# Kernel tuning notes

Hardware: AMD Instinct MI355X
Metric: run time of the kernel (lower is better)

## Reference

```python
import jax, jax.numpy as jnp
import numpy as np

N, T = 1024, 32
D_FEAT, GATE_START, GATE_END = 158, 158, 221
D_MODEL = 256
T_NHEAD, S_NHEAD = 4, 2
BETA = 5.0
LN_EPS = 1e-5


def _ln(x, g, b):
    mu = jnp.mean(x, axis=-1, keepdims=True)
    var = jnp.mean(jnp.square(x - mu), axis=-1, keepdims=True)
    return (x - mu) * jax.lax.rsqrt(var + LN_EPS) * g + b


def _pos_enc(t, d):
    pos = jnp.arange(t, dtype=jnp.float32)[:, None]
    div = jnp.exp(jnp.arange(0, d, 2, dtype=jnp.float32) * (-np.log(10000.0) / d))
    pe = jnp.zeros((t, d), dtype=jnp.float32)
    pe = pe.at[:, 0::2].set(jnp.sin(pos * div))
    pe = pe.at[:, 1::2].set(jnp.cos(pos * div))
    return pe


def _mha(xn, qw, kw, vw, nhead, temperature):
    # xn: [B, S, D] (already layer-normed); attention over axis S
    B, S, D = xn.shape
    dh = D // nhead
    q = (xn @ qw.T).reshape(B, S, nhead, dh)
    k = (xn @ kw.T).reshape(B, S, nhead, dh)
    v = (xn @ vw.T).reshape(B, S, nhead, dh)
    scores = jnp.einsum('bshd,bthd->bhst', q, k) / temperature
    a = jax.nn.softmax(scores, axis=-1)
    return jnp.einsum('bhst,bthd->bshd', a, v).reshape(B, S, D)


def _block(x, qw, kw, vw, n1g, n1b, n2g, n2b, f1w, f1b, f2w, f2b, nhead, temperature):
    xn = _ln(x, n1g, n1b)
    xt = xn + _mha(xn, qw, kw, vw, nhead, temperature)
    xt = _ln(xt, n2g, n2b)
    ffn = jnp.maximum(xt @ f1w.T + f1b, 0.0) @ f2w.T + f2b
    return xt + ffn


def _forward(x, gate_w, gate_b, proj_w, proj_b,
             tq, tk, tv, tn1g, tn1b, tn2g, tn2b, tf1w, tf1b, tf2w, tf2b,
             sq, sk, sv, sn1g, sn1b, sn2g, sn2b, sf1w, sf1b, sf2w, sf2b,
             temp_w, out_w, out_b):
    src = x[:, :, :GATE_START]                     # [N, T, d_feat]
    gate_in = x[:, -1, GATE_START:GATE_END]        # [N, d_gate]
    gate = D_FEAT * jax.nn.softmax((gate_in @ gate_w.T + gate_b) / BETA, axis=-1)
    src = src * gate[:, None, :]
    z = src @ proj_w.T + proj_b                    # [N, T, d_model]
    z = z + _pos_enc(z.shape[1], D_MODEL)
    # TAttention: attend over time, unscaled scores (temperature=1)
    z = _block(z, tq, tk, tv, tn1g, tn1b, tn2g, tn2b, tf1w, tf1b, tf2w, tf2b,
               T_NHEAD, 1.0)
    # SAttention: attend over stocks, temperature = sqrt(d_model/nhead)
    zs = _block(z.swapaxes(0, 1), sq, sk, sv, sn1g, sn1b, sn2g, sn2b,
                sf1w, sf1b, sf2w, sf2b, S_NHEAD, float(np.sqrt(D_MODEL / S_NHEAD)))
    z = zs.swapaxes(0, 1)                          # [N, T, d_model]
    # TemporalAttention pooling
    h = z @ temp_w.T
    lam = jax.nn.softmax(jnp.einsum('ntd,nd->nt', h, h[:, -1, :]), axis=1)
    pooled = jnp.einsum('nt,ntd->nd', lam, z)
    return (pooled @ out_w.T + out_b).squeeze(-1)  # [N]


def setup_inputs() -> dict:
    key = jax.random.key(0)
    ks = iter(jax.random.split(key, 32))
    s = 0.02
    d, f, g = D_MODEL, D_FEAT, GATE_END - GATE_START
    inp = {
        'x': jax.random.normal(next(ks), (N, T, GATE_END), dtype=jnp.float32),
        'gate_w': jax.random.normal(next(ks), (f, g)) * s,
        'gate_b': jnp.zeros((f,)),
        'proj_w': jax.random.normal(next(ks), (d, f)) * s,
        'proj_b': jnp.zeros((d,)),
        'tq': jax.random.normal(next(ks), (d, d)) * s,
        'tk': jax.random.normal(next(ks), (d, d)) * s,
        'tv': jax.random.normal(next(ks), (d, d)) * s,
        'tn1g': jnp.ones((d,)), 'tn1b': jnp.zeros((d,)),
        'tn2g': jnp.ones((d,)), 'tn2b': jnp.zeros((d,)),
        'tf1w': jax.random.normal(next(ks), (d, d)) * s, 'tf1b': jnp.zeros((d,)),
        'tf2w': jax.random.normal(next(ks), (d, d)) * s, 'tf2b': jnp.zeros((d,)),
        'sq': jax.random.normal(next(ks), (d, d)) * s,
        'sk': jax.random.normal(next(ks), (d, d)) * s,
        'sv': jax.random.normal(next(ks), (d, d)) * s,
        'sn1g': jnp.ones((d,)), 'sn1b': jnp.zeros((d,)),
        'sn2g': jnp.ones((d,)), 'sn2b': jnp.zeros((d,)),
        'sf1w': jax.random.normal(next(ks), (d, d)) * s, 'sf1b': jnp.zeros((d,)),
        'sf2w': jax.random.normal(next(ks), (d, d)) * s, 'sf2b': jnp.zeros((d,)),
        'temp_w': jax.random.normal(next(ks), (d, d)) * s,
        'out_w': jax.random.normal(next(ks), (1, d)) * s,
        'out_b': jnp.zeros((1,)),
    }
    return {k: v.astype(jnp.float32) for k, v in inp.items()}


def reference(x, gate_w, gate_b, proj_w, proj_b,
              tq, tk, tv, tn1g, tn1b, tn2g, tn2b, tf1w, tf1b, tf2w, tf2b,
              sq, sk, sv, sn1g, sn1b, sn2g, sn2b, sf1w, sf1b, sf2w, sf2b,
              temp_w, out_w, out_b):
    return _forward(x, gate_w, gate_b, proj_w, proj_b,
                    tq, tk, tv, tn1g, tn1b, tn2g, tn2b, tf1w, tf1b, tf2w, tf2b,
                    sq, sk, sv, sn1g, sn1b, sn2g, sn2b, sf1w, sf1b, sf2w, sf2b,
                    temp_w, out_w, out_b)
```

## Files before the change

kernel.cpp:

```cpp
#include <hip/hip_runtime.h>
#include <math.h>

#define NB   1024
#define TSEQ 32
#define DM   256
#define DF   158
#define GDIM 63
#define XROW 221

typedef unsigned short u16;
typedef __attribute__((ext_vector_type(8))) __bf16 bf16x8;
typedef __attribute__((ext_vector_type(4))) float f32x4;
#define MFMA16(a,b,c) __builtin_amdgcn_mfma_f32_16x16x32_bf16(a,b,c,0,0,0)

#define MODE_PROJ 0
#define MODE_QKVT 1
#define MODE_QKVS 2
#define MODE_TEMP 3

__device__ __forceinline__ u16 f2bf(float f){
  union { float f; unsigned int u; } c; c.f = f;
  unsigned int u = c.u;
  u += 0x7fffu + ((u >> 16) & 1u);
  return (u16)(u >> 16);
}

__device__ __forceinline__ void gl2lds16(const u16* g, u16* lds_wave_base, int lane){
#if __has_builtin(__builtin_amdgcn_global_load_lds)
  __builtin_amdgcn_global_load_lds(
      (const __attribute__((address_space(1))) unsigned int*)g,
      (__attribute__((address_space(3))) unsigned int*)lds_wave_base,
      16, 0, 0);
#else
  *reinterpret_cast<uint4*>(lds_wave_base + lane * 8) =
      *reinterpret_cast<const uint4*>(g);
#endif
}

__device__ __forceinline__ void ln_rows32(float* buf, int stride,
                                          const float* __restrict__ g,
                                          const float* __restrict__ b,
                                          int tid)
{
  const int s = tid >> 3, j = tid & 7;
  float* row = buf + s * stride;
  float sum = 0.f, sq = 0.f;
  #pragma unroll
  for (int k = 0; k < DM; k += 8){
    float v = row[k + j];
    sum += v; sq += v * v;
  }
  #pragma unroll
  for (int o = 1; o < 8; o <<= 1){
    sum += __shfl_xor(sum, o);
    sq  += __shfl_xor(sq, o);
  }
  const float mu  = sum * (1.f / DM);
  const float var = sq * (1.f / DM) - mu * mu;
  const float rs  = rsqrtf(var + 1e-5f);
  #pragma unroll
  for (int k = 0; k < DM; k += 8){
    float v = row[k + j];
    row[k + j] = (v - mu) * rs * g[k + j] + b[k + j];
  }
}

#define WB_TOT 770048

__global__ __launch_bounds__(256) void kConvAll(
    const float* __restrict__ tq, const float* __restrict__ tk, const float* __restrict__ tv,
    const float* __restrict__ sq, const float* __restrict__ sk, const float* __restrict__ sv,
    const float* __restrict__ tf1, const float* __restrict__ tf2,
    const float* __restrict__ sf1, const float* __restrict__ sf2,
    const float* __restrict__ tw, const float* __restrict__ pw,
    u16* __restrict__ WB)
{
  int i = blockIdx.x * 256 + threadIdx.x;
  if (i >= WB_TOT) return;
  if (i < 720896){
    int j = i >> 16, o = i & 65535;
    const float* s;
    switch (j){
      case 0: s = tq; break;  case 1: s = tk; break;  case 2: s = tv; break;
      case 3: s = sq; break;  case 4: s = sk; break;  case 5: s = sv; break;
      case 6: s = tf1; break; case 7: s = tf2; break;
      case 8: s = sf1; break; case 9: s = sf2; break;
      default: s = tw; break;
    }
    WB[i] = f2bf(s[o]);
  } else {
    int k = i - 720896;
    int row = k / 192, col = k - row * 192;
    WB[i] = (col < DF) ? f2bf(pw[row * DF + col]) : (u16)0;
  }
}


__global__ __launch_bounds__(256) void kGateSrc(
    const float* __restrict__ x,
    const float* __restrict__ gate_w, const float* __restrict__ gate_b,
    u16* __restrict__ SRC)
{
  __shared__ float s_gate[DF];
  __shared__ float s_gi[GDIM];
  const int tid = threadIdx.x;
  const int n = blockIdx.x;

  if (tid < GDIM) s_gi[tid] = x[(n * TSEQ + (TSEQ - 1)) * XROW + DF + tid];
  __syncthreads();
  float logit = 0.f;
  if (tid < DF){
    logit = gate_b[tid];
    const float* __restrict__ wr = gate_w + tid * GDIM;
    for (int g = 0; g < GDIM; ++g) logit += s_gi[g] * wr[g];
    logit *= 0.2f;
    s_gate[tid] = logit;
  }
  __syncthreads();
  {
    float mx = -1e30f;
    for (int f = 0; f < DF; ++f) mx = fmaxf(mx, s_gate[f]);
    float sm = 0.f;
    for (int f = 0; f < DF; ++f) sm += __expf(s_gate[f] - mx);
    __syncthreads();
    if (tid < DF) s_gate[tid] = (float)DF * __expf(logit - mx) / sm;
  }
  __syncthreads();

  for (int e = tid; e < TSEQ * 192; e += 256){
    int t = e / 192, f = e - t * 192;
    float v = 0.f;
    if (f < DF) v = x[(n * TSEQ + t) * XROW + f] * s_gate[f];
    SRC[(size_t)(n * TSEQ + t) * 192 + f] = f2bf(v);
  }
}


__global__ __launch_bounds__(256) void gemm_bf16(
    const u16* __restrict__ A, const u16* __restrict__ B,
    const int K, const int mode,
    const float* __restrict__ bias,
    float* __restrict__ outf,
    u16* __restrict__ ob0, u16* __restrict__ ob1, u16* __restrict__ ob2)
{
  __shared__ alignas(16) u16 sA[128 * 64];
  __shared__ alignas(16) u16 sB[128 * 64];
  const int tid = threadIdx.x;
  const int wv = tid >> 6, lane = tid & 63;
  const int wr = wv >> 1, wc = wv & 1;
  const int quad = lane >> 4, lc = lane & 15;
  const int n0 = blockIdx.y * 128;
  const bool tmaj = (mode == MODE_QKVS);
  const int tt = tmaj ? (blockIdx.x & 31) : 0;
  const int nb = tmaj ? (blockIdx.x >> 5) : 0;
  const int m0 = tmaj ? 0 : blockIdx.x * 128;

  f32x4 acc[4][4];
  #pragma unroll
  for (int i = 0; i < 4; ++i)
    #pragma unroll
    for (int j = 0; j < 4; ++j) acc[i][j] = (f32x4){0.f,0.f,0.f,0.f};

  for (int kt = 0; kt < K; kt += 64){
    __syncthreads();
    #pragma unroll
    for (int j = 0; j < 4; ++j){
      int c = wv * 64 + lane + j * 256;
      int row = c >> 3, blk = c & 7;
      int arow = tmaj ? ((nb * 128 + row) * 32 + tt) : (m0 + row);
      gl2lds16(A + (size_t)arow * K + kt + ((blk ^ (row & 7)) * 8),
               &sA[(wv * 64 + j * 256) * 8], lane);
      gl2lds16(B + (size_t)(n0 + row) * K + kt + ((blk ^ (row & 7)) * 8),
               &sB[(wv * 64 + j * 256) * 8], lane);
    }
    __syncthreads();
    #pragma unroll
    for (int kc = 0; kc < 2; ++kc){
      const int sw = ((kc * 4 + quad) ^ (lc & 7)) * 8;
      bf16x8 a[4], b[4];
      #pragma unroll
      for (int i = 0; i < 4; ++i){
        a[i] = *reinterpret_cast<const bf16x8*>(&sA[(wr * 64 + i * 16 + lc) * 64 + sw]);
        b[i] = *reinterpret_cast<const bf16x8*>(&sB[(wc * 64 + i * 16 + lc) * 64 + sw]);
      }
      #pragma unroll
      for (int i = 0; i < 4; ++i)
        #pragma unroll
        for (int j = 0; j < 4; ++j)
          acc[i][j] = MFMA16(a[i], b[j], acc[i][j]);
    }
  }

  const int rb = wr * 64 + quad * 4;
  const int cb = wc * 64 + lc;

  if (mode == MODE_PROJ){
    #pragma unroll
    for (int i = 0; i < 4; ++i)
      #pragma unroll
      for (int r = 0; r < 4; ++r){
        int row = m0 + rb + i * 16 + r;
        float ft = (float)(row & 31);
        #pragma unroll
        for (int j = 0; j < 4; ++j){
          int col = n0 + cb + j * 16;
          float div = __expf((float)(col & ~1) * -0.035977892f);
          float ang = ft * div;
          float pe = (col & 1) ? __cosf(ang) : __sinf(ang);
          outf[(size_t)row * 256 + col] = acc[i][j][r] + bias[col] + pe;
        }
      }
  } else if (mode == MODE_QKVT){
    #pragma unroll
    for (int i = 0; i < 4; ++i)
      #pragma unroll
      for (int r = 0; r < 4; ++r){
        int row = m0 + rb + i * 16 + r;
        #pragma unroll
        for (int j = 0; j < 4; ++j){
          int col = n0 + cb + j * 16;
          int sel = col >> 8, c = col & 255;
          u16 v = f2bf(acc[i][j][r]);
          if (sel == 0)      ob0[(size_t)row * 256 + c] = v;
          else if (sel == 1) ob1[(size_t)row * 256 + c] = v;
          else {
            int h = c >> 6, dd = c & 63;
            ob2[(((size_t)(row >> 5) * 4 + h) * 64 + dd) * 32 + (row & 31)] = v;
          }
        }
      }
  } else if (mode == MODE_QKVS){
    #pragma unroll
    for (int i = 0; i < 4; ++i)
      #pragma unroll
      for (int r = 0; r < 4; ++r){
        int rl = rb + i * 16 + r;
        int n = nb * 128 + rl;
        #pragma unroll
        for (int j = 0; j < 4; ++j){
          int col = n0 + cb + j * 16;
          int sel = col >> 8, c = col & 255;
          u16 v = f2bf(acc[i][j][r]);
          if (sel == 0)      ob0[((size_t)tt * NB + n) * 256 + c] = v;
          else if (sel == 1) ob1[((size_t)tt * NB + n) * 256 + c] = v;
          else {
            int h = c >> 7, dd = c & 127;
            ob2[(((size_t)tt * 2 + h) * 128 + dd) * NB + n] = v;
          }
        }
      }
  } else {
    #pragma unroll
    for (int i = 0; i < 4; ++i)
      #pragma unroll
      for (int r = 0; r < 4; ++r){
        int row = m0 + rb + i * 16 + r;
        #pragma unroll
        for (int j = 0; j < 4; ++j){
          int col = n0 + cb + j * 16;
          outf[(size_t)row * 256 + col] = acc[i][j][r];
        }
      }
  }
}


__global__ __launch_bounds__(256) void kLN(
    const float* __restrict__ X, const float* __restrict__ g,
    const float* __restrict__ b,
    u16* __restrict__ Xb, float* __restrict__ Xf)
{
  __shared__ float s_z[32 * DM];
  const int tid = threadIdx.x;
  const size_t base = (size_t)blockIdx.x * (32 * DM);
  for (int e = tid; e < 32 * DM; e += 256) s_z[e] = X[base + e];
  __syncthreads();
  ln_rows32(s_z, DM, g, b, tid);
  __syncthreads();
  for (int e = tid; e < 32 * DM; e += 256){
    float v = s_z[e];
    Xb[base + e] = f2bf(v);
    Xf[base + e] = v;
  }
}


__global__ __launch_bounds__(512) void kFFN(
    const float* __restrict__ X,
    const float* __restrict__ lg, const float* __restrict__ lb,
    const u16* __restrict__ w1, const float* __restrict__ b1,
    const u16* __restrict__ w2, const float* __restrict__ b2,
    float* __restrict__ outf, u16* __restrict__ obdual)
{
  __shared__ alignas(16) u16 sAB[24576];
  __shared__ alignas(16) u16 s_h1[128 * 256];
  __shared__ float s_mu[128], s_rs[128];
  __shared__ float s_lg[256], s_lb[256], s_b1[256], s_b2[256];

  const int tid = threadIdx.x;
  const int wv = tid >> 6, lane = tid & 63;
  const int quad = lane >> 4, lc = lane & 15;
  const int m0 = blockIdx.x * 128;
  const int m0w = (wv >> 1) * 32;
  const int n0w = (wv & 1) * 128;
  u16* sA = sAB;
  u16* sB = sAB + 8192;

  if (tid < 256){
    s_lg[tid] = lg[tid]; s_lb[tid] = lb[tid];
    s_b1[tid] = b1[tid]; s_b2[tid] = b2[tid];
  }

  {
    const int row = tid >> 2, j = tid & 3;
    const float4* xr = reinterpret_cast<const float4*>(X + (size_t)(m0 + row) * 256);
    float sum = 0.f, sq = 0.f;
    #pragma unroll
    for (int k = 0; k < 16; ++k){
      float4 v = xr[j + 4 * k];
      sum += v.x + v.y + v.z + v.w;
      sq  += v.x*v.x + v.y*v.y + v.z*v.z + v.w*v.w;
    }
    sum += __shfl_xor(sum, 1); sq += __shfl_xor(sq, 1);
    sum += __shfl_xor(sum, 2); sq += __shfl_xor(sq, 2);
    if (j == 0){
      float mu = sum * (1.f / 256.f);
      s_mu[row] = mu;
      s_rs[row] = rsqrtf(sq * (1.f / 256.f) - mu * mu + 1e-5f);
    }
  }
  __syncthreads();

  f32x4 acc[2][8];
  #pragma unroll
  for (int mt = 0; mt < 2; ++mt)
    #pragma unroll
    for (int j = 0; j < 8; ++j) acc[mt][j] = (f32x4){0.f,0.f,0.f,0.f};

  for (int kt = 0; kt < 4; ++kt){
    __syncthreads();
    {
      const int row = tid >> 2, c0 = (tid & 3) * 16;
      const float mu = s_mu[row], rs = s_rs[row];
      const float* xp = X + (size_t)(m0 + row) * 256 + kt * 64 + c0;
      u16 v16[16];
      #pragma unroll
      for (int k = 0; k < 4; ++k){
        float4 v = *reinterpret_cast<const float4*>(xp + 4 * k);
        int col = kt * 64 + c0 + 4 * k;
        v16[4*k+0] = f2bf((v.x - mu) * rs * s_lg[col+0] + s_lb[col+0]);
        v16[4*k+1] = f2bf((v.y - mu) * rs * s_lg[col+1] + s_lb[col+1]);
        v16[4*k+2] = f2bf((v.z - mu) * rs * s_lg[col+2] + s_lb[col+2]);
        v16[4*k+3] = f2bf((v.w - mu) * rs * s_lg[col+3] + s_lb[col+3]);
      }
      int b0 = c0 >> 3;
      *reinterpret_cast<uint4*>(&sA[row * 64 + ((b0    ) ^ (row & 7)) * 8]) = *reinterpret_cast<uint4*>(&v16[0]);
      *reinterpret_cast<uint4*>(&sA[row * 64 + ((b0 + 1) ^ (row & 7)) * 8]) = *reinterpret_cast<uint4*>(&v16[8]);
    }
    #pragma unroll
    for (int i = 0; i < 4; ++i){
      int c = tid + i * 512;
      int row = c >> 3, blk = c & 7;
      *reinterpret_cast<uint4*>(&sB[row * 64 + (blk ^ (row & 7)) * 8]) =
        *reinterpret_cast<const uint4*>(w1 + (size_t)row * 256 + kt * 64 + blk * 8);
    }
    __syncthreads();
    #pragma unroll
    for (int kc = 0; kc < 2; ++kc){
      const int sw = ((kc * 4 + quad) ^ (lc & 7)) * 8;
      bf16x8 a[2], b[8];
      #pragma unroll
      for (int mt = 0; mt < 2; ++mt)
        a[mt] = *reinterpret_cast<const bf16x8*>(&sA[(m0w + mt * 16 + lc) * 64 + sw]);
      #pragma unroll
      for (int j = 0; j < 8; ++j)
        b[j] = *reinterpret_cast<const bf16x8*>(&sB[(n0w + j * 16 + lc) * 64 + sw]);
      #pragma unroll
      for (int mt = 0; mt < 2; ++mt)
        #pragma unroll
        for (int j = 0; j < 8; ++j)
          acc[mt][j] = MFMA16(a[mt], b[j], acc[mt][j]);
    }
  }
  __syncthreads();

  #pragma unroll
  for (int mt = 0; mt < 2; ++mt)
    #pragma unroll
    for (int r = 0; r < 4; ++r){
      int row = m0w + mt * 16 + quad * 4 + r;
      #pragma unroll
      for (int j = 0; j < 8; ++j){
        int col = n0w + j * 16 + lc;
        u16 v = f2bf(fmaxf(acc[mt][j][r] + s_b1[col], 0.f));
        s_h1[row * 256 + (((col >> 3) ^ (row & 31)) << 3) + (col & 7)] = v;
      }
    }

  #pragma unroll
  for (int mt = 0; mt < 2; ++mt)
    #pragma unroll
    for (int j = 0; j < 8; ++j) acc[mt][j] = (f32x4){0.f,0.f,0.f,0.f};

  for (int kt = 0; kt < 4; ++kt){
    __syncthreads();
    #pragma unroll
    for (int i = 0; i < 4; ++i){
      int c = tid + i * 512;
      int row = c >> 3, blk = c & 7;
      *reinterpret_cast<uint4*>(&sAB[row * 64 + (blk ^ (row & 7)) * 8]) =
        *reinterpret_cast<const uint4*>(w2 + (size_t)row * 256 + kt * 64 + blk * 8);
    }
    __syncthreads();
    #pragma unroll
    for (int kc = 0; kc < 2; ++kc){
      const int sw = ((kc * 4 + quad) ^ (lc & 7)) * 8;
      bf16x8 a[2], b[8];
      #pragma unroll
      for (int mt = 0; mt < 2; ++mt){
        int row = m0w + mt * 16 + lc;
        int cb = kt * 8 + kc * 4 + quad;
        a[mt] = *reinterpret_cast<const bf16x8*>(
            &s_h1[row * 256 + ((cb ^ (row & 31)) << 3)]);
      }
      #pragma unroll
      for (int j = 0; j < 8; ++j)
        b[j] = *reinterpret_cast<const bf16x8*>(&sAB[(n0w + j * 16 + lc) * 64 + sw]);
      #pragma unroll
      for (int mt = 0; mt < 2; ++mt)
        #pragma unroll
        for (int j = 0; j < 8; ++j)
          acc[mt][j] = MFMA16(a[mt], b[j], acc[mt][j]);
    }
  }

  #pragma unroll
  for (int mt = 0; mt < 2; ++mt)
    #pragma unroll
    for (int r = 0; r < 4; ++r){
      int rowl = m0w + mt * 16 + quad * 4 + r;
      const float mu = s_mu[rowl], rs = s_rs[rowl];
      size_t base = (size_t)(m0 + rowl) * 256;
      #pragma unroll
      for (int j = 0; j < 8; ++j){
        int col = n0w + j * 16 + lc;
        float xn = (X[base + col] - mu) * rs * s_lg[col] + s_lb[col];
        float v = acc[mt][j][r] + s_b2[col] + xn;
        outf[base + col] = v;
        if (obdual) obdual[base + col] = f2bf(v);
      }
    }
}


__global__ __launch_bounds__(256) void kAttnT(
    const u16* __restrict__ Qt, const u16* __restrict__ Kt,
    const u16* __restrict__ VtT, const float* __restrict__ XN1f,
    float* __restrict__ X2)
{
  __shared__ alignas(16) u16 sQ[4][32 * 72];
  __shared__ alignas(16) u16 sK[4][32 * 72];
  __shared__ alignas(16) u16 sV[4][64 * 40];
  __shared__ alignas(16) u16 sP[4][32 * 40];

  const int tid = threadIdx.x;
  const int wv = tid >> 6, lane = tid & 63;
  const int quad = lane >> 4, lc = lane & 15;
  const int n = blockIdx.x;
  const int h = wv;
  const f32x4 zero4 = {0.f, 0.f, 0.f, 0.f};

  #pragma unroll
  for (int i = 0; i < 4; ++i){
    int c = lane + 64 * i;
    int row = c >> 3, blk = c & 7;
    *reinterpret_cast<uint4*>(&sQ[wv][row * 72 + blk * 8]) =
      *reinterpret_cast<const uint4*>(&Qt[((size_t)n * 32 + row) * 256 + h * 64 + blk * 8]);
    *reinterpret_cast<uint4*>(&sK[wv][row * 72 + blk * 8]) =
      *reinterpret_cast<const uint4*>(&Kt[((size_t)n * 32 + row) * 256 + h * 64 + blk * 8]);
    int rv = c >> 2, bv = c & 3;
    *reinterpret_cast<uint4*>(&sV[wv][rv * 40 + bv * 8]) =
      *reinterpret_cast<const uint4*>(&VtT[(((size_t)n * 4 + h) * 64 + rv) * 32 + bv * 8]);
  }
  __syncthreads();

  f32x4 s[2][2];
  #pragma unroll
  for (int mt = 0; mt < 2; ++mt)
    #pragma unroll
    for (int ct = 0; ct < 2; ++ct) s[mt][ct] = zero4;
  #pragma unroll
  for (int kc = 0; kc < 2; ++kc){
    bf16x8 aq[2], bk[2];
    #pragma unroll
    for (int mt = 0; mt < 2; ++mt)
      aq[mt] = *reinterpret_cast<const bf16x8*>(&sQ[wv][(mt * 16 + lc) * 72 + kc * 32 + quad * 8]);
    #pragma unroll
    for (int ct = 0; ct < 2; ++ct)
      bk[ct] = *reinterpret_cast<const bf16x8*>(&sK[wv][(ct * 16 + lc) * 72 + kc * 32 + quad * 8]);
    #pragma unroll
    for (int mt = 0; mt < 2; ++mt)
      #pragma unroll
      for (int ct = 0; ct < 2; ++ct)
        s[mt][ct] = MFMA16(aq[mt], bk[ct], s[mt][ct]);
  }

  #pragma unroll
  for (int mt = 0; mt < 2; ++mt){
    #pragma unroll
    for (int r = 0; r < 4; ++r){
      float v0 = s[mt][0][r], v1 = s[mt][1][r];
      float mx = fmaxf(v0, v1);
      #pragma unroll
      for (int msk = 1; msk < 16; msk <<= 1) mx = fmaxf(mx, __shfl_xor(mx, msk));
      float p0 = __expf(v0 - mx), p1 = __expf(v1 - mx);
      float sm = p0 + p1;
      #pragma unroll
      for (int msk = 1; msk < 16; msk <<= 1) sm += __shfl_xor(sm, msk);
      float inv = 1.f / sm;
      sP[wv][(mt * 16 + quad * 4 + r) * 40 + lc]      = f2bf(p0 * inv);
      sP[wv][(mt * 16 + quad * 4 + r) * 40 + lc + 16] = f2bf(p1 * inv);
    }
  }
  __syncthreads();

  #pragma unroll
  for (int mt = 0; mt < 2; ++mt){
    bf16x8 ap = *reinterpret_cast<const bf16x8*>(&sP[wv][(mt * 16 + lc) * 40 + quad * 8]);
    #pragma unroll
    for (int ct = 0; ct < 4; ++ct){
      bf16x8 bv = *reinterpret_cast<const bf16x8*>(&sV[wv][(ct * 16 + lc) * 40 + quad * 8]);
      f32x4 o = MFMA16(ap, bv, zero4);
      #pragma unroll
      for (int r = 0; r < 4; ++r){
        int t = mt * 16 + quad * 4 + r;
        size_t idx = ((size_t)n * 32 + t) * 256 + h * 64 + ct * 16 + lc;
        X2[idx] = XN1f[idx] + o[r];
      }
    }
  }
}


__global__ __launch_bounds__(256) void kB2_flash_mfma(
    const u16* __restrict__ Qh, const u16* __restrict__ Kh,
    const u16* __restrict__ VT, const float* __restrict__ XNs,
    float* __restrict__ XT)
{
  __shared__ alignas(16) u16 s_k[64 * 136];
  __shared__ alignas(16) u16 s_vt[128 * 72];
  __shared__ alignas(16) u16 s_p[4][32 * 72];

  const int tid = threadIdx.x;
  const int wv = tid >> 6, lane = tid & 63;
  const int quad = lane >> 4, lc = lane & 15;
  const int t = blockIdx.x >> 1, h = blockIdx.x & 1;
  const int n0 = blockIdx.y * 128;
  const float c_exp2 = 0.12752887f;
  const int qb = n0 + wv * 32;

  bf16x8 qf[2][4];
  #pragma unroll
  for (int mt = 0; mt < 2; ++mt){
    const u16* qp = Qh + ((size_t)(t * NB + qb + mt * 16 + lc)) * DM + h * 128 + quad * 8;
    #pragma unroll
    for (int kc = 0; kc < 4; ++kc)
      qf[mt][kc] = *reinterpret_cast<const bf16x8*>(qp + kc * 32);
  }

  f32x4 o[2][8];
  #pragma unroll
  for (int mt = 0; mt < 2; ++mt)
    #pragma unroll
    for (int f = 0; f < 8; ++f) o[mt][f] = (f32x4){0.f, 0.f, 0.f, 0.f};
  float l_acc[2][4] = {{0.f,0.f,0.f,0.f},{0.f,0.f,0.f,0.f}};

  const u16* kbase  = Kh + (size_t)t * NB * DM + h * 128;
  const u16* vtbase = VT + (size_t)(t * 2 + h) * 128 * NB;
  u16* pw = s_p[wv];

  for (int j0 = 0; j0 < NB; j0 += 64){
    __syncthreads();
    #pragma unroll
    for (int it = 0; it < 4; ++it){
      int c = tid + it * 256;
      int row = c >> 4, part = c & 15;
      *reinterpret_cast<uint4*>(&s_k[row * 136 + part * 8]) =
        *reinterpret_cast<const uint4*>(kbase + (size_t)(j0 + row) * DM + part * 8);
      int rv = c >> 3, pv = c & 7;
      *reinterpret_cast<uint4*>(&s_vt[rv * 72 + pv * 8]) =
        *reinterpret_cast<const uint4*>(vtbase + (size_t)rv * NB + j0 + pv * 8);
    }
    __syncthreads();

    f32x4 s[2][4];
    #pragma unroll
    for (int mt = 0; mt < 2; ++mt)
      #pragma unroll
      for (int nt = 0; nt < 4; ++nt) s[mt][nt] = (f32x4){0.f,0.f,0.f,0.f};
    #pragma unroll
    for (int kc = 0; kc < 4; ++kc){
      #pragma unroll
      for (int nt = 0; nt < 4; ++nt){
        bf16x8 bk = *reinterpret_cast<const bf16x8*>(
            &s_k[(lc + 16 * nt) * 136 + kc * 32 + quad * 8]);
        #pragma unroll
        for (int mt = 0; mt < 2; ++mt)
          s[mt][nt] = MFMA16(qf[mt][kc], bk, s[mt][nt]);
      }
    }

    #pragma unroll
    for (int mt = 0; mt < 2; ++mt)
      #pragma unroll
      for (int nt = 0; nt < 4; ++nt)
        #pragma unroll
        for (int r = 0; r < 4; ++r){
          float p = exp2f(s[mt][nt][r] * c_exp2);
          l_acc[mt][r] += p;
          pw[(mt * 16 + quad * 4 + r) * 72 + lc + 16 * nt] = f2bf(p);
        }

    bf16x8 ap[2][2];
    #pragma unroll
    for (int mt = 0; mt < 2; ++mt){
      ap[mt][0] = *reinterpret_cast<const bf16x8*>(&pw[(mt * 16 + lc) * 72 + quad * 8]);
      ap[mt][1] = *reinterpret_cast<const bf16x8*>(&pw[(mt * 16 + lc) * 72 + 32 + quad * 8]);
    }
    #pragma unroll
    for (int f = 0; f < 8; ++f){
      bf16x8 bv0 = *reinterpret_cast<const bf16x8*>(&s_vt[(lc + 16 * f) * 72 + quad * 8]);
      bf16x8 bv1 = *reinterpret_cast<const bf16x8*>(&s_vt[(lc + 16 * f) * 72 + 32 + quad * 8]);
      #pragma unroll
      for (int mt = 0; mt < 2; ++mt){
        o[mt][f] = MFMA16(ap[mt][0], bv0, o[mt][f]);
        o[mt][f] = MFMA16(ap[mt][1], bv1, o[mt][f]);
      }
    }
  }

  #pragma unroll
  for (int mt = 0; mt < 2; ++mt)
    #pragma unroll
    for (int r = 0; r < 4; ++r){
      #pragma unroll
      for (int msk = 1; msk < 16; msk <<= 1)
        l_acc[mt][r] += __shfl_xor(l_acc[mt][r], msk);
    }

  #pragma unroll
  for (int mt = 0; mt < 2; ++mt)
    #pragma unroll
    for (int r = 0; r < 4; ++r){
      float linv = 1.f / l_acc[mt][r];
      int row = qb + mt * 16 + quad * 4 + r;
      size_t xnb = ((size_t)row * TSEQ + t) * DM + h * 128 + lc;
      size_t xtb = ((size_t)t * NB + row) * DM + h * 128 + lc;
      #pragma unroll
      for (int f = 0; f < 8; ++f)
        XT[xtb + f * 16] = XNs[xnb + f * 16] + o[mt][f][r] * linv;
    }
}


__global__ __launch_bounds__(256) void kC_pool(
    const float* __restrict__ Ht, const float* __restrict__ ZS,
    const float* __restrict__ out_w, const float* __restrict__ out_b,
    float* __restrict__ out)
{
  __shared__ float s_z[32 * DM];
  __shared__ float s_h[32 * 260];
  __shared__ float s_sc[32];
  __shared__ float s_red[4];
  const int tid = threadIdx.x;
  const int n = blockIdx.x;

  for (int e = tid; e < 32 * DM; e += 256){
    int i = e >> 8, dd = e & 255;
    s_h[i * 260 + dd] = Ht[((size_t)i * NB + n) * DM + dd];
    s_z[e]            = ZS[((size_t)i * NB + n) * DM + dd];
  }
  __syncthreads();

  {
    const int s = tid >> 3, j = tid & 7;
    float acc = 0.f;
    #pragma unroll
    for (int k = 0; k < DM; k += 8) acc += s_h[s * 260 + k + j] * s_h[31 * 260 + k + j];
    #pragma unroll
    for (int o = 1; o < 8; o <<= 1) acc += __shfl_xor(acc, o);
    if (j == 0) s_sc[s] = acc;
  }
  __syncthreads();

  float mx = -1e30f;
  #pragma unroll
  for (int s = 0; s < 32; ++s) mx = fmaxf(mx, s_sc[s]);
  float sm = 0.f;
  #pragma unroll
  for (int s = 0; s < 32; ++s) sm += __expf(s_sc[s] - mx);
  const float inv = 1.f / sm;

  const int d = tid;
  float pooled = 0.f;
  #pragma unroll
  for (int s = 0; s < 32; ++s) pooled += __expf(s_sc[s] - mx) * inv * s_z[s * DM + d];

  float val = pooled * out_w[d];
  #pragma unroll
  for (int o = 1; o < 64; o <<= 1) val += __shfl_xor(val, o);
  if ((tid & 63) == 0) s_red[tid >> 6] = val;
  __syncthreads();
  if (tid == 0) out[n] = s_red[0] + s_red[1] + s_red[2] + s_red[3] + out_b[0];
}


extern "C" void kernel_launch(void* const* d_in, const int* in_sizes, int n_in,
                              void* d_out, int out_size, void* d_ws, size_t ws_size,
                              hipStream_t stream)
{
  const float* x      = (const float*)d_in[0];
  const float* gate_w = (const float*)d_in[1];
  const float* gate_b = (const float*)d_in[2];
  const float* proj_w = (const float*)d_in[3];
  const float* proj_b = (const float*)d_in[4];
  const float* tq   = (const float*)d_in[5];
  const float* tk   = (const float*)d_in[6];
  const float* tv   = (const float*)d_in[7];
  const float* tn1g = (const float*)d_in[8];
  const float* tn1b = (const float*)d_in[9];
  const float* tn2g = (const float*)d_in[10];
  const float* tn2b = (const float*)d_in[11];
  const float* tf1w = (const float*)d_in[12];
  const float* tf1b = (const float*)d_in[13];
  const float* tf2w = (const float*)d_in[14];
  const float* tf2b = (const float*)d_in[15];
  const float* sq   = (const float*)d_in[16];
  const float* sk   = (const float*)d_in[17];
  const float* sv   = (const float*)d_in[18];
  const float* sn1g = (const float*)d_in[19];
  const float* sn1b = (const float*)d_in[20];
  const float* sn2g = (const float*)d_in[21];
  const float* sn2b = (const float*)d_in[22];
  const float* sf1w = (const float*)d_in[23];
  const float* sf1b = (const float*)d_in[24];
  const float* sf2w = (const float*)d_in[25];
  const float* sf2b = (const float*)d_in[26];
  const float* temp_w = (const float*)d_in[27];
  const float* out_w  = (const float*)d_in[28];
  const float* out_b  = (const float*)d_in[29];

  float* W = (float*)d_ws;
  const size_t F = (size_t)NB * TSEQ * DM;

  float* Z  = W;
  float* XF = W + F;
  u16* U0 = (u16*)(W + 2 * F);
  u16* U1 = (u16*)(W + 2 * F) + F;
  u16* U2 = (u16*)(W + 3 * F);
  u16* U3 = (u16*)(W + 3 * F) + F;
  u16* SRC = (u16*)(W + 4 * F);
  u16* WB  = (u16*)(W + 4 * F + 3145728 + 4096);

  kConvAll<<<(WB_TOT + 255) / 256, 256, 0, stream>>>(
      tq, tk, tv, sq, sk, sv, tf1w, tf2w, sf1w, sf2w, temp_w, proj_w, WB);
  kGateSrc<<<NB, 256, 0, stream>>>(x, gate_w, gate_b, SRC);
  gemm_bf16<<<dim3(256, 2), 256, 0, stream>>>(SRC, WB + 720896, 192, MODE_PROJ,
      proj_b, Z, nullptr, nullptr, nullptr);
  kLN<<<NB, 256, 0, stream>>>(Z, tn1g, tn1b, U0, XF);
  gemm_bf16<<<dim3(256, 6), 256, 0, stream>>>(U0, WB, 256, MODE_QKVT,
      nullptr, nullptr, U1, U2, U3);
  kAttnT<<<NB, 256, 0, stream>>>(U1, U2, U3, XF, Z);
  kFFN<<<256, 512, 0, stream>>>(Z, tn2g, tn2b, WB + 393216, tf1b,
      WB + 458752, tf2b, Z, nullptr);
  kLN<<<NB, 256, 0, stream>>>(Z, sn1g, sn1b, U2, XF);
  gemm_bf16<<<dim3(256, 6), 256, 0, stream>>>(U2, WB + 196608, 256, MODE_QKVS,
      nullptr, nullptr, U3, U1, U0);
  kB2_flash_mfma<<<dim3(64, 8), 256, 0, stream>>>(U3, U1, U0, XF, Z);
  kFFN<<<256, 512, 0, stream>>>(Z, sn2g, sn2b, WB + 524288, sf1b,
      WB + 589824, sf2b, Z, U0);
  gemm_bf16<<<dim3(256, 2), 256, 0, stream>>>(U0, WB + 655360, 256, MODE_TEMP,
      nullptr, XF, nullptr, nullptr, nullptr);
  kC_pool<<<NB, 256, 0, stream>>>(XF, Z, out_w, out_b, (float*)d_out);
}
```

Baseline: 497.7 us.

## Split flash attention key tile across two wave groups with LDS reduction

The stock-axis flash attention kernel now launches 512 threads per block. Each of two wave groups handles half of every 64-key tile, and their partial outputs and softmax sums are combined through shared memory at the end. This doubles waves per block to raise occupancy and latency hiding, at the cost of an extra LDS reduction and more barriers. It also replaces round-to-nearest bf16 conversion of probabilities with truncation, which is cheaper but slightly less accurate.

```diff
diff --git a/kernel.cpp b/kernel.cpp
--- a/kernel.cpp
+++ b/kernel.cpp
@@ -23,6 +23,11 @@
   unsigned int u = c.u;
   u += 0x7fffu + ((u >> 16) & 1u);
   return (u16)(u >> 16);
+}
+
+__device__ __forceinline__ u16 f2bf_t(float f){
+  union { float f; unsigned int u; } c; c.f = f;
+  return (u16)(c.u >> 16);
 }
 
 __device__ __forceinline__ void gl2lds16(const u16* g, u16* lds_wave_base, int lane){
@@ -542,22 +547,24 @@
 }
 
 
-__global__ __launch_bounds__(256) void kB2_flash_mfma(
+__global__ __launch_bounds__(512) void kB2_flash_mfma(
     const u16* __restrict__ Qh, const u16* __restrict__ Kh,
     const u16* __restrict__ VT, const float* __restrict__ XNs,
     float* __restrict__ XT)
 {
-  __shared__ alignas(16) u16 s_k[64 * 136];
-  __shared__ alignas(16) u16 s_vt[128 * 72];
-  __shared__ alignas(16) u16 s_p[4][32 * 72];
+  __shared__ alignas(16) u16 smem[28160];
+  u16* s_k  = smem;
+  u16* s_vt = smem + 8704;
+  u16* s_p  = smem + 17920;
 
   const int tid = threadIdx.x;
   const int wv = tid >> 6, lane = tid & 63;
+  const int wq = wv & 3, wk = wv >> 2;
   const int quad = lane >> 4, lc = lane & 15;
   const int t = blockIdx.x >> 1, h = blockIdx.x & 1;
   const int n0 = blockIdx.y * 128;
   const float c_exp2 = 0.12752887f;
-  const int qb = n0 + wv * 32;
+  const int qb = n0 + wq * 32;
 
   bf16x8 qf[2][4];
   #pragma unroll
@@ -577,13 +584,13 @@
 
   const u16* kbase  = Kh + (size_t)t * NB * DM + h * 128;
   const u16* vtbase = VT + (size_t)(t * 2 + h) * 128 * NB;
-  u16* pw = s_p[wv];
+  u16* pw = s_p + wv * 1280;
 
   for (int j0 = 0; j0 < NB; j0 += 64){
     __syncthreads();
     #pragma unroll
-    for (int it = 0; it < 4; ++it){
-      int c = tid + it * 256;
+    for (int it = 0; it < 2; ++it){
+      int c = tid + it * 512;
       int row = c >> 4, part = c & 15;
       *reinterpret_cast<uint4*>(&s_k[row * 136 + part * 8]) =
         *reinterpret_cast<const uint4*>(kbase + (size_t)(j0 + row) * DM + part * 8);
@@ -593,17 +600,17 @@
     }
     __syncthreads();
 
-    f32x4 s[2][4];
+    f32x4 s[2][2];
     #pragma unroll
     for (int mt = 0; mt < 2; ++mt)
       #pragma unroll
-      for (int nt = 0; nt < 4; ++nt) s[mt][nt] = (f32x4){0.f,0.f,0.f,0.f};
+      for (int nt = 0; nt < 2; ++nt) s[mt][nt] = (f32x4){0.f,0.f,0.f,0.f};
     #pragma unroll
     for (int kc = 0; kc < 4; ++kc){
       #pragma unroll
-      for (int nt = 0; nt < 4; ++nt){
+      for (int nt = 0; nt < 2; ++nt){
         bf16x8 bk = *reinterpret_cast<const bf16x8*>(
-            &s_k[(lc + 16 * nt) * 136 + kc * 32 + quad * 8]);
+            &s_k[(lc + 16 * nt + 32 * wk) * 136 + kc * 32 + quad * 8]);
         #pragma unroll
         for (int mt = 0; mt < 2; ++mt)
           s[mt][nt] = MFMA16(qf[mt][kc], bk, s[mt][nt]);
@@ -613,53 +620,98 @@
     #pragma unroll
     for (int mt = 0; mt < 2; ++mt)
       #pragma unroll
-      for (int nt = 0; nt < 4; ++nt)
+      for (int nt = 0; nt < 2; ++nt)
         #pragma unroll
         for (int r = 0; r < 4; ++r){
           float p = exp2f(s[mt][nt][r] * c_exp2);
           l_acc[mt][r] += p;
-          pw[(mt * 16 + quad * 4 + r) * 72 + lc + 16 * nt] = f2bf(p);
+          pw[(mt * 16 + quad * 4 + r) * 40 + lc + 16 * nt] = f2bf_t(p);
         }
 
-    bf16x8 ap[2][2];
-    #pragma unroll
-    for (int mt = 0; mt < 2; ++mt){
-      ap[mt][0] = *reinterpret_cast<const bf16x8*>(&pw[(mt * 16 + lc) * 72 + quad * 8]);
-      ap[mt][1] = *reinterpret_cast<const bf16x8*>(&pw[(mt * 16 + lc) * 72 + 32 + quad * 8]);
-    }
+    bf16x8 ap[2];
+    #pragma unroll
+    for (int mt = 0; mt < 2; ++mt)
+      ap[mt] = *reinterpret_cast<const bf16x8*>(&pw[(mt * 16 + lc) * 40 + quad * 8]);
     #pragma unroll
     for (int f = 0; f < 8; ++f){
-      bf16x8 bv0 = *reinterpret_cast<const bf16x8*>(&s_vt[(lc + 16 * f) * 72 + quad * 8]);
-      bf16x8 bv1 = *reinterpret_cast<const bf16x8*>(&s_vt[(lc + 16 * f) * 72 + 32 + quad * 8]);
-      #pragma unroll
-      for (int mt = 0; mt < 2; ++mt){
-        o[mt][f] = MFMA16(ap[mt][0], bv0, o[mt][f]);
-        o[mt][f] = MFMA16(ap[mt][1], bv1, o[mt][f]);
-      }
-    }
-  }
-
-  #pragma unroll
-  for (int mt = 0; mt < 2; ++mt)
+      bf16x8 bv = *reinterpret_cast<const bf16x8*>(
+          &s_vt[(lc + 16 * f) * 72 + 32 * wk + quad * 8]);
+      #pragma unroll
+      for (int mt = 0; mt < 2; ++mt)
+        o[mt][f] = MFMA16(ap[mt], bv, o[mt][f]);
+    }
+  }
+
+  float* fo = (float*)smem;
+  float* fl = (float*)smem + 8192;
+
+  __syncthreads();
+  if (wk == 1){
+    int base = (wq * 64 + lane) * 32;
+    #pragma unroll
+    for (int f = 0; f < 8; ++f)
+      #pragma unroll
+      for (int r = 0; r < 4; ++r) fo[base + f * 4 + r] = o[0][f][r];
+    int lb = (wq * 64 + lane) * 8;
+    #pragma unroll
+    for (int mt = 0; mt < 2; ++mt)
+      #pragma unroll
+      for (int r = 0; r < 4; ++r) fl[lb + mt * 4 + r] = l_acc[mt][r];
+  }
+  __syncthreads();
+  if (wk == 0){
+    int base = (wq * 64 + lane) * 32;
+    #pragma unroll
+    for (int f = 0; f < 8; ++f)
+      #pragma unroll
+      for (int r = 0; r < 4; ++r) o[0][f][r] += fo[base + f * 4 + r];
+    int lb = (wq * 64 + lane) * 8;
+    #pragma unroll
+    for (int mt = 0; mt < 2; ++mt)
+      #pragma unroll
+      for (int r = 0; r < 4; ++r){
+        l_acc[mt][r] += fl[lb + mt * 4 + r];
+        #pragma unroll
+        for (int msk = 1; msk < 16; msk <<= 1)
+          l_acc[mt][r] += __shfl_xor(l_acc[mt][r], msk);
+      }
     #pragma unroll
     for (int r = 0; r < 4; ++r){
-      #pragma unroll
-      for (int msk = 1; msk < 16; msk <<= 1)
-        l_acc[mt][r] += __shfl_xor(l_acc[mt][r], msk);
-    }
-
-  #pragma unroll
-  for (int mt = 0; mt < 2; ++mt)
-    #pragma unroll
-    for (int r = 0; r < 4; ++r){
-      float linv = 1.f / l_acc[mt][r];
-      int row = qb + mt * 16 + quad * 4 + r;
+      float linv = 1.f / l_acc[0][r];
+      int row = qb + quad * 4 + r;
       size_t xnb = ((size_t)row * TSEQ + t) * DM + h * 128 + lc;
       size_t xtb = ((size_t)t * NB + row) * DM + h * 128 + lc;
       #pragma unroll
       for (int f = 0; f < 8; ++f)
-        XT[xtb + f * 16] = XNs[xnb + f * 16] + o[mt][f][r] * linv;
-    }
+        XT[xtb + f * 16] = XNs[xnb + f * 16] + o[0][f][r] * linv;
+    }
+  }
+  __syncthreads();
+  if (wk == 1){
+    int base = (wq * 64 + lane) * 32;
+    #pragma unroll
+    for (int f = 0; f < 8; ++f)
+      #pragma unroll
+      for (int r = 0; r < 4; ++r) fo[base + f * 4 + r] = o[1][f][r];
+  }
+  __syncthreads();
+  if (wk == 0){
+    int base = (wq * 64 + lane) * 32;
+    #pragma unroll
+    for (int f = 0; f < 8; ++f)
+      #pragma unroll
+      for (int r = 0; r < 4; ++r) o[1][f][r] += fo[base + f * 4 + r];
+    #pragma unroll
+    for (int r = 0; r < 4; ++r){
+      float linv = 1.f / l_acc[1][r];
+      int row = qb + 16 + quad * 4 + r;
+      size_t xnb = ((size_t)row * TSEQ + t) * DM + h * 128 + lc;
+      size_t xtb = ((size_t)t * NB + row) * DM + h * 128 + lc;
+      #pragma unroll
+      for (int f = 0; f < 8; ++f)
+        XT[xtb + f * 16] = XNs[xnb + f * 16] + o[1][f][r] * linv;
+    }
+  }
 }
 
 
@@ -776,7 +828,7 @@
   kLN<<<NB, 256, 0, stream>>>(Z, sn1g, sn1b, U2, XF);
   gemm_bf16<<<dim3(256, 6), 256, 0, stream>>>(U2, WB + 196608, 256, MODE_QKVS,
       nullptr, nullptr, U3, U1, U0);
-  kB2_flash_mfma<<<dim3(64, 8), 256, 0, stream>>>(U3, U1, U0, XF, Z);
+  kB2_flash_mfma<<<dim3(64, 8), 512, 0, stream>>>(U3, U1, U0, XF, Z);
   kFFN<<<256, 512, 0, stream>>>(Z, sn2g, sn2b, WB + 524288, sf1b,
       WB + 589824, sf2b, Z, U0);
   gemm_bf16<<<dim3(256, 2), 256, 0, stream>>>(U0, WB + 655360, 256, MODE_TEMP,
```

Result: faster. 478.8 us (median of 2 runs) (-3.8%).
